# Performance work log

Hardware: AMD Instinct MI355X
Metric: run time of the kernel (lower is better)

## Reference

```python
import jax, jax.numpy as jnp
import numpy as np

B, D, H = 2048, 64, 512  # batch, state dim, vf hidden dim
IS_DIFFUSION = True      # vf output divided by 2.0 as in CNF.forward


def setup_inputs() -> dict:
    key = jax.random.key(0)
    ks = jax.random.split(key, 8)

    def lin(k, fi, fo):
        return jax.random.normal(k, (fi, fo), jnp.float32) / np.float32(np.sqrt(fi))

    return {
        "t": jax.random.uniform(ks[0], (1,), jnp.float32),      # scalar time, kept as [1]
        "x": jax.random.normal(ks[1], (B, D + 1), jnp.float32),  # last col = logp channel
        "W1": lin(ks[2], D + 1, H),
        "b1": jax.random.normal(ks[3], (H,), jnp.float32) * 0.01,
        "W2": lin(ks[4], H, H),
        "b2": jax.random.normal(ks[5], (H,), jnp.float32) * 0.01,
        "W3": lin(ks[6], H, D),
        "b3": jax.random.normal(ks[7], (D,), jnp.float32) * 0.01,
    }


def reference(t, x, W1, b1, W2, b2, W3, b3):
    scale = 2.0 if IS_DIFFUSION else 1.0
    xd = x[..., :-1]  # [B, D] -- drop augmented log-density channel

    def vf_single(xi):  # R^D -> R^D vector field, t and params closed over
        h = jnp.concatenate([xi, t])           # [D+1] (time-conditioned input)
        h = jnp.tanh(h @ W1 + b1)
        h = jnp.tanh(h @ W2 + b2)
        return (h @ W3 + b3) / scale

    dx = jax.vmap(vf_single)(xd)  # [B, D]
    # exact divergence: trace of per-sample Jacobian via reverse-mode (matches torch jacrev)
    div = jax.vmap(lambda xi: jnp.trace(jax.jacrev(vf_single)(xi)))(xd)  # [B]
    return jnp.concatenate([dx, div[:, None]], axis=-1)  # [B, D+1]
```

## Files before the change

kernel.cpp:

```cpp
#include <hip/hip_runtime.h>


constexpr int HD = 512;
constexpr int DD = 64;
constexpr int SB = 8;
constexpr int NB = 2048 / SB;

typedef __attribute__((ext_vector_type(8))) short bf16x8;
typedef __attribute__((ext_vector_type(4))) float f32x4;

__device__ inline unsigned short f2bf(float f) {
    union { float f; unsigned u; } v; v.f = f;
    return (unsigned short)((v.u + 0x7fffu + ((v.u >> 16) & 1u)) >> 16);
}
__device__ inline float fast_tanh(float xx) {
    float e = __expf(2.f * xx);
    return 1.f - 2.f / (e + 1.f);
}

__global__ __launch_bounds__(64) void cnf_pack_kernel(
    const float* __restrict__ W1, const float* __restrict__ W2,
    const float* __restrict__ W3, unsigned short* __restrict__ Bpack)
{
    __shared__ float w1s[64][33];
    __shared__ float w3s[16][65];
    const int b = blockIdx.x;
    const int mat = b >> 9, t = (b >> 4) & 31, kk = b & 15;
    const int l = threadIdx.x;
    const int q = l >> 4, nl = l & 15;
    const int n = t * 16 + nl;
    unsigned short o[8];
    if (mat == 0) {
#pragma unroll
        for (int j = 0; j < 8; ++j) {
            int k = kk * 32 + q * 8 + j;
            o[j] = f2bf(W2[k * HD + n]);
        }
    } else {
        for (int e = l; e < 64 * 32; e += 64) {
            int i = e >> 5, kl = e & 31;
            w1s[i][kl] = W1[i * HD + kk * 32 + kl];
        }
        for (int e = l; e < 16 * 64; e += 64) {
            int nn = e >> 6, i = e & 63;
            w3s[nn][i] = W3[(t * 16 + nn) * DD + i];
        }
        __syncthreads();
#pragma unroll
        for (int j = 0; j < 8; ++j) {
            int kl = q * 8 + j;
            float m = 0.f;
#pragma unroll 8
            for (int i = 0; i < 64; ++i) m += w1s[i][kl] * w3s[nl][i];
            o[j] = f2bf(W2[(kk * 32 + kl) * HD + n] * m);
        }
    }
    uint4 pk;
    pk.x = (unsigned)o[0] | ((unsigned)o[1] << 16);
    pk.y = (unsigned)o[2] | ((unsigned)o[3] << 16);
    pk.z = (unsigned)o[4] | ((unsigned)o[5] << 16);
    pk.w = (unsigned)o[6] | ((unsigned)o[7] << 16);
    reinterpret_cast<uint4*>(Bpack)[b * 64 + l] = pk;
}

__global__ __launch_bounds__(512, 2) void cnf_fused_kernel(
    const float* __restrict__ tptr, const float* __restrict__ x,
    const float* __restrict__ W1, const float* __restrict__ b1,
    const float* __restrict__ b2v, const float* __restrict__ W3,
    const float* __restrict__ b3, const unsigned short* __restrict__ Bpack,
    float* __restrict__ out)
{
    __shared__ float4 xsv[65 * 2];
    __shared__ unsigned short A_lds[16][520];
    __shared__ float4 h2v[HD * 2];
    __shared__ float4 divred[8][2];
    __shared__ float sm_b2[HD];

    const int tid  = threadIdx.x;
    const int s0   = blockIdx.x * SB;
    const int wave = tid >> 6, lane = tid & 63;

    {
        const float tval = tptr[0];
        for (int e = tid; e < SB * 65; e += 512) {
            int s = e / 65, i = e % 65;
            reinterpret_cast<float*>(xsv)[i * SB + s] =
                (i == DD) ? tval : x[(s0 + s) * 65 + i];
        }
        sm_b2[tid] = b2v[tid];
    }
    __syncthreads();

    {
        const int u = tid;
        const float bb = b1[u];
        float2 a0 = {bb, bb}, a1 = {bb, bb}, a2 = {bb, bb}, a3 = {bb, bb};
        for (int ib = 0; ib < 64; ib += 8) {
            float w[8];
#pragma unroll
            for (int qq = 0; qq < 8; ++qq) w[qq] = W1[(ib + qq) * HD + u];
#pragma unroll
            for (int qq = 0; qq < 8; ++qq) {
                float4 p = xsv[2 * (ib + qq)], r = xsv[2 * (ib + qq) + 1];
                a0.x += p.x * w[qq]; a0.y += p.y * w[qq];
                a1.x += p.z * w[qq]; a1.y += p.w * w[qq];
                a2.x += r.x * w[qq]; a2.y += r.y * w[qq];
                a3.x += r.z * w[qq]; a3.y += r.w * w[qq];
            }
        }
        {
            float w = W1[64 * HD + u];
            float4 p = xsv[128], r = xsv[129];
            a0.x += p.x * w; a0.y += p.y * w;
            a1.x += p.z * w; a1.y += p.w * w;
            a2.x += r.x * w; a2.y += r.y * w;
            a3.x += r.z * w; a3.y += r.w * w;
        }
        float h[8] = {fast_tanh(a0.x), fast_tanh(a0.y), fast_tanh(a1.x), fast_tanh(a1.y),
                      fast_tanh(a2.x), fast_tanh(a2.y), fast_tanh(a3.x), fast_tanh(a3.y)};
#pragma unroll
        for (int s = 0; s < 8; ++s) {
            A_lds[s][u]     = f2bf(h[s]);
            A_lds[8 + s][u] = f2bf(1.f - h[s] * h[s]);
        }
    }
    __syncthreads();

    f32x4 cw[4], cg[4];
#pragma unroll
    for (int i = 0; i < 4; ++i) { cw[i] = (f32x4){0,0,0,0}; cg[i] = (f32x4){0,0,0,0}; }
    {
        const unsigned short* arow = &A_lds[lane & 15][0];
        const int aoff = (lane >> 4) * 8;
        const bf16x8* bw = reinterpret_cast<const bf16x8*>(Bpack)
                         + (size_t)(wave * 64) * 64 + lane;
        const bf16x8* bg = bw + 32768;

        bf16x8 pA[16], pB[16];
        auto loadSB = [&](bf16x8* d, int kk) {
#pragma unroll
            for (int i = 0; i < 4; ++i) {
                d[i]      = bw[kk * 64 + i * 1024];
                d[4 + i]  = bg[kk * 64 + i * 1024];
                d[8 + i]  = bw[(kk + 1) * 64 + i * 1024];
                d[12 + i] = bg[(kk + 1) * 64 + i * 1024];
            }
        };
        auto mfmaSB = [&](const bf16x8* d, int kk) {
            bf16x8 af0 = *reinterpret_cast<const bf16x8*>(arow + kk * 32 + aoff);
#pragma unroll
            for (int i = 0; i < 4; ++i)
                cw[i] = __builtin_amdgcn_mfma_f32_16x16x32_bf16(af0, d[i], cw[i], 0, 0, 0);
#pragma unroll
            for (int i = 0; i < 4; ++i)
                cg[i] = __builtin_amdgcn_mfma_f32_16x16x32_bf16(af0, d[4 + i], cg[i], 0, 0, 0);
            bf16x8 af1 = *reinterpret_cast<const bf16x8*>(arow + (kk + 1) * 32 + aoff);
#pragma unroll
            for (int i = 0; i < 4; ++i)
                cw[i] = __builtin_amdgcn_mfma_f32_16x16x32_bf16(af1, d[8 + i], cw[i], 0, 0, 0);
#pragma unroll
            for (int i = 0; i < 4; ++i)
                cg[i] = __builtin_amdgcn_mfma_f32_16x16x32_bf16(af1, d[12 + i], cg[i], 0, 0, 0);
        };

        loadSB(pA, 0);
#pragma unroll
        for (int kb = 0; kb < 8; ++kb) {
            bf16x8* cur = (kb & 1) ? pB : pA;
            bf16x8* nxt = (kb & 1) ? pA : pB;
            if (kb < 7) loadSB(nxt, (kb + 1) * 2);
            mfmaSB(cur, kb * 2);
        }
    }

    {
        const int q = lane >> 4;
        const int src = (lane >= 32) ? lane - 32 : lane;
        float4 dp = {0.f, 0.f, 0.f, 0.f};
#pragma unroll
        for (int i = 0; i < 4; ++i) {
            const int m = wave * 64 + i * 16 + (lane & 15);
            const float bb = sm_b2[m];
            float4 hv;
            hv.x = fast_tanh(cw[i][0] + bb);
            hv.y = fast_tanh(cw[i][1] + bb);
            hv.z = fast_tanh(cw[i][2] + bb);
            hv.w = fast_tanh(cw[i][3] + bb);
            if (lane < 32) h2v[2 * m + q] = hv;
            float h0 = __shfl(hv.x, src), h1s = __shfl(hv.y, src);
            float h2s = __shfl(hv.z, src), h3s = __shfl(hv.w, src);
            dp.x += cg[i][0] * (1.f - h0 * h0);
            dp.y += cg[i][1] * (1.f - h1s * h1s);
            dp.z += cg[i][2] * (1.f - h2s * h2s);
            dp.w += cg[i][3] * (1.f - h3s * h3s);
        }
        if (lane >= 32) {
#pragma unroll
            for (int off = 8; off > 0; off >>= 1) {
                dp.x += __shfl_down(dp.x, off, 16);
                dp.y += __shfl_down(dp.y, off, 16);
                dp.z += __shfl_down(dp.z, off, 16);
                dp.w += __shfl_down(dp.w, off, 16);
            }
            if ((lane & 15) == 0) divred[wave][q - 2] = dp;
        }
    }
    __syncthreads();

    float* opart = reinterpret_cast<float*>(A_lds);

    {
        const int k = lane, part = wave;
        float o[8];
#pragma unroll
        for (int q = 0; q < 8; ++q) o[q] = 0.f;
        const int mb = part * 64;
        for (int mm = 0; mm < 64; mm += 4) {
            float w[4];
#pragma unroll
            for (int q = 0; q < 4; ++q) w[q] = W3[(mb + mm + q) * DD + k];
#pragma unroll
            for (int q = 0; q < 4; ++q) {
                const int m = mb + mm + q;
                float4 ha = h2v[2 * m], hb = h2v[2 * m + 1];
                o[0] += ha.x * w[q]; o[1] += ha.y * w[q];
                o[2] += ha.z * w[q]; o[3] += ha.w * w[q];
                o[4] += hb.x * w[q]; o[5] += hb.y * w[q];
                o[6] += hb.z * w[q]; o[7] += hb.w * w[q];
            }
        }
#pragma unroll
        for (int q = 0; q < 8; ++q) opart[part * 512 + q * 64 + k] = o[q];
    }
    __syncthreads();

    {
        const int s = tid >> 6, k = tid & 63;
        float sum = b3[k];
#pragma unroll
        for (int p = 0; p < 8; ++p) sum += opart[p * 512 + s * 64 + k];
        out[(s0 + s) * 65 + k] = 0.5f * sum;
    }
    if (tid < 8) {
        const int qq = tid >> 2, r = tid & 3;
        float ds = 0.f;
#pragma unroll
        for (int w = 0; w < 8; ++w)
            ds += reinterpret_cast<const float*>(&divred[w][qq])[r];
        out[(s0 + tid) * 65 + DD] = 0.5f * ds;
    }
}

extern "C" void kernel_launch(void* const* d_in, const int* in_sizes, int n_in,
                              void* d_out, int out_size, void* d_ws, size_t ws_size,
                              hipStream_t stream) {
    const float* t  = (const float*)d_in[0];
    const float* x  = (const float*)d_in[1];
    const float* W1 = (const float*)d_in[2];
    const float* b1 = (const float*)d_in[3];
    const float* W2 = (const float*)d_in[4];
    const float* b2 = (const float*)d_in[5];
    const float* W3 = (const float*)d_in[6];
    const float* b3 = (const float*)d_in[7];
    float* out = (float*)d_out;
    unsigned short* Bpack = (unsigned short*)d_ws;

    cnf_pack_kernel<<<1024, 64, 0, stream>>>(W1, W2, W3, Bpack);
    cnf_fused_kernel<<<NB, 512, 0, stream>>>(t, x, W1, b1, b2, W3, b3, Bpack, out);
}
```

Baseline: 97.85 us.

## Split fused CNF kernel into prep, pack, tiled GEMM and epilogue kernels

Result: slower. 105.6 us (+7.9%).

```diff
diff --git a/kernel.cpp b/kernel.cpp
--- a/kernel.cpp
+++ b/kernel.cpp
@@ -4,7 +4,6 @@
 constexpr int HD = 512;
 constexpr int DD = 64;
 constexpr int SB = 8;
-constexpr int NB = 2048 / SB;
 
 typedef __attribute__((ext_vector_type(8))) short bf16x8;
 typedef __attribute__((ext_vector_type(4))) float f32x4;
@@ -18,80 +17,28 @@
     return 1.f - 2.f / (e + 1.f);
 }
 
-__global__ __launch_bounds__(64) void cnf_pack_kernel(
-    const float* __restrict__ W1, const float* __restrict__ W2,
-    const float* __restrict__ W3, unsigned short* __restrict__ Bpack)
-{
-    __shared__ float w1s[64][33];
-    __shared__ float w3s[16][65];
-    const int b = blockIdx.x;
-    const int mat = b >> 9, t = (b >> 4) & 31, kk = b & 15;
-    const int l = threadIdx.x;
-    const int q = l >> 4, nl = l & 15;
-    const int n = t * 16 + nl;
-    unsigned short o[8];
-    if (mat == 0) {
-#pragma unroll
-        for (int j = 0; j < 8; ++j) {
-            int k = kk * 32 + q * 8 + j;
-            o[j] = f2bf(W2[k * HD + n]);
-        }
-    } else {
-        for (int e = l; e < 64 * 32; e += 64) {
-            int i = e >> 5, kl = e & 31;
-            w1s[i][kl] = W1[i * HD + kk * 32 + kl];
-        }
-        for (int e = l; e < 16 * 64; e += 64) {
-            int nn = e >> 6, i = e & 63;
-            w3s[nn][i] = W3[(t * 16 + nn) * DD + i];
-        }
-        __syncthreads();
-#pragma unroll
-        for (int j = 0; j < 8; ++j) {
-            int kl = q * 8 + j;
-            float m = 0.f;
-#pragma unroll 8
-            for (int i = 0; i < 64; ++i) m += w1s[i][kl] * w3s[nl][i];
-            o[j] = f2bf(W2[(kk * 32 + kl) * HD + n] * m);
-        }
-    }
-    uint4 pk;
-    pk.x = (unsigned)o[0] | ((unsigned)o[1] << 16);
-    pk.y = (unsigned)o[2] | ((unsigned)o[3] << 16);
-    pk.z = (unsigned)o[4] | ((unsigned)o[5] << 16);
-    pk.w = (unsigned)o[6] | ((unsigned)o[7] << 16);
-    reinterpret_cast<uint4*>(Bpack)[b * 64 + l] = pk;
-}
-
-__global__ __launch_bounds__(512, 2) void cnf_fused_kernel(
+__global__ __launch_bounds__(512) void cnf_prep_kernel(
     const float* __restrict__ tptr, const float* __restrict__ x,
     const float* __restrict__ W1, const float* __restrict__ b1,
-    const float* __restrict__ b2v, const float* __restrict__ W3,
-    const float* __restrict__ b3, const unsigned short* __restrict__ Bpack,
-    float* __restrict__ out)
+    const float* __restrict__ W3,
+    unsigned short* __restrict__ Apack,
+    float* __restrict__ Mws)
 {
     __shared__ float4 xsv[65 * 2];
-    __shared__ unsigned short A_lds[16][520];
-    __shared__ float4 h2v[HD * 2];
-    __shared__ float4 divred[8][2];
-    __shared__ float sm_b2[HD];
-
-    const int tid  = threadIdx.x;
-    const int s0   = blockIdx.x * SB;
-    const int wave = tid >> 6, lane = tid & 63;
-
-    {
-        const float tval = tptr[0];
-        for (int e = tid; e < SB * 65; e += 512) {
-            int s = e / 65, i = e % 65;
-            reinterpret_cast<float*>(xsv)[i * SB + s] =
-                (i == DD) ? tval : x[(s0 + s) * 65 + i];
-        }
-        sm_b2[tid] = b2v[tid];
-    }
-    __syncthreads();
-
-    {
+    __shared__ float w1b[64][8];
+    const int tid = threadIdx.x;
+
+    if (blockIdx.x < 256) {
+        const int s0 = blockIdx.x * SB;
+        {
+            const float tval = tptr[0];
+            for (int e = tid; e < SB * 65; e += 512) {
+                int s = e / 65, i = e % 65;
+                reinterpret_cast<float*>(xsv)[i * SB + s] =
+                    (i == DD) ? tval : x[(s0 + s) * 65 + i];
+            }
+        }
+        __syncthreads();
         const int u = tid;
         const float bb = b1[u];
         float2 a0 = {bb, bb}, a1 = {bb, bb}, a2 = {bb, bb}, a3 = {bb, bb};
@@ -118,96 +65,175 @@
         }
         float h[8] = {fast_tanh(a0.x), fast_tanh(a0.y), fast_tanh(a1.x), fast_tanh(a1.y),
                       fast_tanh(a2.x), fast_tanh(a2.y), fast_tanh(a3.x), fast_tanh(a3.y)};
+        unsigned short* Ah = Apack;
+        unsigned short* Ad = Apack + (size_t)2048 * HD;
 #pragma unroll
         for (int s = 0; s < 8; ++s) {
-            A_lds[s][u]     = f2bf(h[s]);
-            A_lds[8 + s][u] = f2bf(1.f - h[s] * h[s]);
+            Ah[(size_t)(s0 + s) * HD + u] = f2bf(h[s]);
+            Ad[(size_t)(s0 + s) * HD + u] = f2bf(1.f - h[s] * h[s]);
+        }
+    } else {
+        const int kb = (blockIdx.x - 256) * 8;
+        {
+            int i = tid >> 3, kq = tid & 7;
+            w1b[i][kq] = W1[i * HD + kb + kq];
+        }
+        __syncthreads();
+        const int n = tid;
+        float m8[8] = {0.f, 0.f, 0.f, 0.f, 0.f, 0.f, 0.f, 0.f};
+        for (int i = 0; i < 64; i += 4) {
+            float4 w3v = *reinterpret_cast<const float4*>(W3 + n * DD + i);
+#pragma unroll
+            for (int q = 0; q < 4; ++q) {
+                float wv = (q == 0) ? w3v.x : (q == 1) ? w3v.y : (q == 2) ? w3v.z : w3v.w;
+                float4 a = *reinterpret_cast<const float4*>(&w1b[i + q][0]);
+                float4 c = *reinterpret_cast<const float4*>(&w1b[i + q][4]);
+                m8[0] += a.x * wv; m8[1] += a.y * wv; m8[2] += a.z * wv; m8[3] += a.w * wv;
+                m8[4] += c.x * wv; m8[5] += c.y * wv; m8[6] += c.z * wv; m8[7] += c.w * wv;
+            }
+        }
+#pragma unroll
+        for (int j = 0; j < 8; ++j) Mws[(size_t)(kb + j) * HD + n] = m8[j];
+    }
+}
+
+__global__ __launch_bounds__(512) void cnf_pack_kernel(
+    const float* __restrict__ W2, const float* __restrict__ Mws,
+    unsigned short* __restrict__ Bpack)
+{
+    const int b = blockIdx.x * 8 + (threadIdx.x >> 6);
+    const int mat = b >> 9, t = (b >> 4) & 31, kk = b & 15;
+    const int l = threadIdx.x & 63;
+    const int q = l >> 4, nl = l & 15;
+    const int n = t * 16 + nl;
+    unsigned short o[8];
+#pragma unroll
+    for (int j = 0; j < 8; ++j) {
+        int k = kk * 32 + q * 8 + j;
+        float w = W2[k * HD + n];
+        if (mat) w *= Mws[(size_t)k * HD + n];
+        o[j] = f2bf(w);
+    }
+    uint4 pk;
+    pk.x = (unsigned)o[0] | ((unsigned)o[1] << 16);
+    pk.y = (unsigned)o[2] | ((unsigned)o[3] << 16);
+    pk.z = (unsigned)o[4] | ((unsigned)o[5] << 16);
+    pk.w = (unsigned)o[6] | ((unsigned)o[7] << 16);
+    reinterpret_cast<uint4*>(Bpack)[b * 64 + l] = pk;
+}
+
+__global__ __launch_bounds__(256) void cnf_gemm_kernel(
+    const unsigned short* __restrict__ Apack,
+    const unsigned short* __restrict__ Bpack,
+    float* __restrict__ C)
+{
+    const int b = blockIdx.x;
+    const int g  = b >> 7;
+    const int rt = (b >> 3) & 15;
+    const int ct = b & 7;
+    const int tid = threadIdx.x, wave = tid >> 6, lane = tid & 63;
+    const int row0 = rt * 128 + wave * 32;
+
+    const bf16x8* A  = reinterpret_cast<const bf16x8*>(Apack) + (size_t)g * 2048 * 64;
+    const bf16x8* Bf = reinterpret_cast<const bf16x8*>(Bpack)
+                     + (size_t)((g * 32 + ct * 4) * 16) * 64 + lane;
+    const int a0 = (row0 + (lane & 15)) * 64 + (lane >> 4);
+    const int a1 = a0 + 16 * 64;
+
+    f32x4 acc[2][4];
+#pragma unroll
+    for (int rg = 0; rg < 2; ++rg)
+#pragma unroll
+        for (int i = 0; i < 4; ++i) acc[rg][i] = (f32x4){0.f, 0.f, 0.f, 0.f};
+
+    bf16x8 p0[12], p1[12], p2[12];
+    auto loadSB = [&](bf16x8* d, int kk) {
+        d[0] = A[a0 + kk * 4];
+        d[1] = A[a1 + kk * 4];
+#pragma unroll
+        for (int i = 0; i < 4; ++i) d[2 + i] = Bf[(i * 16 + kk) * 64];
+        d[6] = A[a0 + (kk + 1) * 4];
+        d[7] = A[a1 + (kk + 1) * 4];
+#pragma unroll
+        for (int i = 0; i < 4; ++i) d[8 + i] = Bf[(i * 16 + kk + 1) * 64];
+    };
+    auto mfmaSB = [&](const bf16x8* d) {
+#pragma unroll
+        for (int i = 0; i < 4; ++i) {
+            acc[0][i] = __builtin_amdgcn_mfma_f32_16x16x32_bf16(d[0], d[2 + i], acc[0][i], 0, 0, 0);
+            acc[1][i] = __builtin_amdgcn_mfma_f32_16x16x32_bf16(d[1], d[2 + i], acc[1][i], 0, 0, 0);
+        }
+#pragma unroll
+        for (int i = 0; i < 4; ++i) {
+            acc[0][i] = __builtin_amdgcn_mfma_f32_16x16x32_bf16(d[6], d[8 + i], acc[0][i], 0, 0, 0);
+            acc[1][i] = __builtin_amdgcn_mfma_f32_16x16x32_bf16(d[7], d[8 + i], acc[1][i], 0, 0, 0);
+        }
+    };
+
+    loadSB(p0, 0);
+    loadSB(p1, 2);
+#pragma unroll
+    for (int kb = 0; kb < 8; ++kb) {
+        const int c3 = kb % 3, n3 = (kb + 2) % 3;
+        bf16x8* cur = (c3 == 0) ? p0 : (c3 == 1) ? p1 : p2;
+        bf16x8* nxt = (n3 == 0) ? p0 : (n3 == 1) ? p1 : p2;
+        if (kb < 6) loadSB(nxt, (kb + 2) * 2);
+        mfmaSB(cur);
+    }
+
+    float* Cg = C + (size_t)g * 2048 * HD;
+    const int colb = ct * 64 + (lane & 15);
+#pragma unroll
+    for (int rg = 0; rg < 2; ++rg) {
+        const int rbase = row0 + rg * 16 + (lane >> 4) * 4;
+#pragma unroll
+        for (int i = 0; i < 4; ++i) {
+#pragma unroll
+            for (int reg = 0; reg < 4; ++reg)
+                Cg[(size_t)(rbase + reg) * HD + colb + i * 16] = acc[rg][i][reg];
+        }
+    }
+}
+
+__global__ __launch_bounds__(512) void cnf_out_kernel(
+    const float* __restrict__ C,
+    const float* __restrict__ b2v, const float* __restrict__ W3,
+    const float* __restrict__ b3, float* __restrict__ out)
+{
+    __shared__ float4 h2v[HD * 2];
+    __shared__ float opart[8 * 512];
+    __shared__ float divred[8][8];
+    const int tid = threadIdx.x;
+    const int s0 = blockIdx.x * SB;
+    const int wave = tid >> 6, lane = tid & 63;
+    const float* C1 = C;
+    const float* C2 = C + (size_t)2048 * HD;
+
+    {
+        const int m = tid;
+        const float bb = b2v[m];
+        float hh[8], dp[8];
+#pragma unroll
+        for (int s = 0; s < 8; ++s) {
+            float c1 = C1[(size_t)(s0 + s) * HD + m];
+            float c2 = C2[(size_t)(s0 + s) * HD + m];
+            float h = fast_tanh(c1 + bb);
+            hh[s] = h;
+            dp[s] = c2 * (1.f - h * h);
+        }
+        h2v[2 * m]     = (float4){hh[0], hh[1], hh[2], hh[3]};
+        h2v[2 * m + 1] = (float4){hh[4], hh[5], hh[6], hh[7]};
+#pragma unroll
+        for (int s = 0; s < 8; ++s) {
+#pragma unroll
+            for (int off = 32; off > 0; off >>= 1) dp[s] += __shfl_down(dp[s], off);
+        }
+        if (lane == 0) {
+#pragma unroll
+            for (int s = 0; s < 8; ++s) divred[wave][s] = dp[s];
         }
     }
     __syncthreads();
-
-    f32x4 cw[4], cg[4];
-#pragma unroll
-    for (int i = 0; i < 4; ++i) { cw[i] = (f32x4){0,0,0,0}; cg[i] = (f32x4){0,0,0,0}; }
-    {
-        const unsigned short* arow = &A_lds[lane & 15][0];
-        const int aoff = (lane >> 4) * 8;
-        const bf16x8* bw = reinterpret_cast<const bf16x8*>(Bpack)
-                         + (size_t)(wave * 64) * 64 + lane;
-        const bf16x8* bg = bw + 32768;
-
-        bf16x8 pA[16], pB[16];
-        auto loadSB = [&](bf16x8* d, int kk) {
-#pragma unroll
-            for (int i = 0; i < 4; ++i) {
-                d[i]      = bw[kk * 64 + i * 1024];
-                d[4 + i]  = bg[kk * 64 + i * 1024];
-                d[8 + i]  = bw[(kk + 1) * 64 + i * 1024];
-                d[12 + i] = bg[(kk + 1) * 64 + i * 1024];
-            }
-        };
-        auto mfmaSB = [&](const bf16x8* d, int kk) {
-            bf16x8 af0 = *reinterpret_cast<const bf16x8*>(arow + kk * 32 + aoff);
-#pragma unroll
-            for (int i = 0; i < 4; ++i)
-                cw[i] = __builtin_amdgcn_mfma_f32_16x16x32_bf16(af0, d[i], cw[i], 0, 0, 0);
-#pragma unroll
-            for (int i = 0; i < 4; ++i)
-                cg[i] = __builtin_amdgcn_mfma_f32_16x16x32_bf16(af0, d[4 + i], cg[i], 0, 0, 0);
-            bf16x8 af1 = *reinterpret_cast<const bf16x8*>(arow + (kk + 1) * 32 + aoff);
-#pragma unroll
-            for (int i = 0; i < 4; ++i)
-                cw[i] = __builtin_amdgcn_mfma_f32_16x16x32_bf16(af1, d[8 + i], cw[i], 0, 0, 0);
-#pragma unroll
-            for (int i = 0; i < 4; ++i)
-                cg[i] = __builtin_amdgcn_mfma_f32_16x16x32_bf16(af1, d[12 + i], cg[i], 0, 0, 0);
-        };
-
-        loadSB(pA, 0);
-#pragma unroll
-        for (int kb = 0; kb < 8; ++kb) {
-            bf16x8* cur = (kb & 1) ? pB : pA;
-            bf16x8* nxt = (kb & 1) ? pA : pB;
-            if (kb < 7) loadSB(nxt, (kb + 1) * 2);
-            mfmaSB(cur, kb * 2);
-        }
-    }
-
-    {
-        const int q = lane >> 4;
-        const int src = (lane >= 32) ? lane - 32 : lane;
-        float4 dp = {0.f, 0.f, 0.f, 0.f};
-#pragma unroll
-        for (int i = 0; i < 4; ++i) {
-            const int m = wave * 64 + i * 16 + (lane & 15);
-            const float bb = sm_b2[m];
-            float4 hv;
-            hv.x = fast_tanh(cw[i][0] + bb);
-            hv.y = fast_tanh(cw[i][1] + bb);
-            hv.z = fast_tanh(cw[i][2] + bb);
-            hv.w = fast_tanh(cw[i][3] + bb);
-            if (lane < 32) h2v[2 * m + q] = hv;
-            float h0 = __shfl(hv.x, src), h1s = __shfl(hv.y, src);
-            float h2s = __shfl(hv.z, src), h3s = __shfl(hv.w, src);
-            dp.x += cg[i][0] * (1.f - h0 * h0);
-            dp.y += cg[i][1] * (1.f - h1s * h1s);
-            dp.z += cg[i][2] * (1.f - h2s * h2s);
-            dp.w += cg[i][3] * (1.f - h3s * h3s);
-        }
-        if (lane >= 32) {
-#pragma unroll
-            for (int off = 8; off > 0; off >>= 1) {
-                dp.x += __shfl_down(dp.x, off, 16);
-                dp.y += __shfl_down(dp.y, off, 16);
-                dp.z += __shfl_down(dp.z, off, 16);
-                dp.w += __shfl_down(dp.w, off, 16);
-            }
-            if ((lane & 15) == 0) divred[wave][q - 2] = dp;
-        }
-    }
-    __syncthreads();
-
-    float* opart = reinterpret_cast<float*>(A_lds);
 
     {
         const int k = lane, part = wave;
@@ -242,11 +268,9 @@
         out[(s0 + s) * 65 + k] = 0.5f * sum;
     }
     if (tid < 8) {
-        const int qq = tid >> 2, r = tid & 3;
         float ds = 0.f;
 #pragma unroll
-        for (int w = 0; w < 8; ++w)
-            ds += reinterpret_cast<const float*>(&divred[w][qq])[r];
+        for (int w = 0; w < 8; ++w) ds += divred[w][tid];
         out[(s0 + tid) * 65 + DD] = 0.5f * ds;
     }
 }
@@ -263,8 +287,14 @@
     const float* W3 = (const float*)d_in[6];
     const float* b3 = (const float*)d_in[7];
     float* out = (float*)d_out;
+
     unsigned short* Bpack = (unsigned short*)d_ws;
-
-    cnf_pack_kernel<<<1024, 64, 0, stream>>>(W1, W2, W3, Bpack);
-    cnf_fused_kernel<<<NB, 512, 0, stream>>>(t, x, W1, b1, b2, W3, b3, Bpack, out);
-}
+    float*          Mws   = (float*)((char*)d_ws + (1 << 20));
+    unsigned short* Apack = (unsigned short*)((char*)d_ws + (2 << 20));
+    float*          Cws   = (float*)((char*)d_ws + (6 << 20));
+
+    cnf_prep_kernel<<<320, 512, 0, stream>>>(t, x, W1, b1, W3, Apack, Mws);
+    cnf_pack_kernel<<<128, 512, 0, stream>>>(W2, Mws, Bpack);
+    cnf_gemm_kernel<<<256, 256, 0, stream>>>(Apack, Bpack, Cws);
+    cnf_out_kernel<<<256, 512, 0, stream>>>(Cws, b2, W3, b3, out);
+}
```

## Merge weight-packing kernel into main kernel with cooperative grid sync

Applied to the files above, without the earlier changes.

Measured after the change: 193.6 us. 97.9% more time.

```diff
diff --git a/kernel.cpp b/kernel.cpp
--- a/kernel.cpp
+++ b/kernel.cpp
@@ -1,4 +1,7 @@
 #include <hip/hip_runtime.h>
+#include <hip/hip_cooperative_groups.h>
+
+namespace cg = cooperative_groups;
 
 
 constexpr int HD = 512;
@@ -18,67 +21,28 @@
     return 1.f - 2.f / (e + 1.f);
 }
 
-__global__ __launch_bounds__(64) void cnf_pack_kernel(
-    const float* __restrict__ W1, const float* __restrict__ W2,
-    const float* __restrict__ W3, unsigned short* __restrict__ Bpack)
-{
-    __shared__ float w1s[64][33];
-    __shared__ float w3s[16][65];
-    const int b = blockIdx.x;
-    const int mat = b >> 9, t = (b >> 4) & 31, kk = b & 15;
-    const int l = threadIdx.x;
-    const int q = l >> 4, nl = l & 15;
-    const int n = t * 16 + nl;
-    unsigned short o[8];
-    if (mat == 0) {
-#pragma unroll
-        for (int j = 0; j < 8; ++j) {
-            int k = kk * 32 + q * 8 + j;
-            o[j] = f2bf(W2[k * HD + n]);
-        }
-    } else {
-        for (int e = l; e < 64 * 32; e += 64) {
-            int i = e >> 5, kl = e & 31;
-            w1s[i][kl] = W1[i * HD + kk * 32 + kl];
-        }
-        for (int e = l; e < 16 * 64; e += 64) {
-            int nn = e >> 6, i = e & 63;
-            w3s[nn][i] = W3[(t * 16 + nn) * DD + i];
-        }
-        __syncthreads();
-#pragma unroll
-        for (int j = 0; j < 8; ++j) {
-            int kl = q * 8 + j;
-            float m = 0.f;
-#pragma unroll 8
-            for (int i = 0; i < 64; ++i) m += w1s[i][kl] * w3s[nl][i];
-            o[j] = f2bf(W2[(kk * 32 + kl) * HD + n] * m);
-        }
-    }
-    uint4 pk;
-    pk.x = (unsigned)o[0] | ((unsigned)o[1] << 16);
-    pk.y = (unsigned)o[2] | ((unsigned)o[3] << 16);
-    pk.z = (unsigned)o[4] | ((unsigned)o[5] << 16);
-    pk.w = (unsigned)o[6] | ((unsigned)o[7] << 16);
-    reinterpret_cast<uint4*>(Bpack)[b * 64 + l] = pk;
-}
-
-__global__ __launch_bounds__(512, 2) void cnf_fused_kernel(
+
+__global__ __launch_bounds__(512, 2) void cnf_mega_kernel(
     const float* __restrict__ tptr, const float* __restrict__ x,
     const float* __restrict__ W1, const float* __restrict__ b1,
-    const float* __restrict__ b2v, const float* __restrict__ W3,
-    const float* __restrict__ b3, const unsigned short* __restrict__ Bpack,
-    float* __restrict__ out)
+    const float* __restrict__ W2, const float* __restrict__ b2v,
+    const float* __restrict__ W3, const float* __restrict__ b3,
+    unsigned short* Bpack, float* __restrict__ out)
 {
     __shared__ float4 xsv[65 * 2];
     __shared__ unsigned short A_lds[16][520];
     __shared__ float4 h2v[HD * 2];
     __shared__ float4 divred[8][2];
     __shared__ float sm_b2[HD];
+    __shared__ float w1s[64][65];
+    __shared__ float w3s[16][68];
 
     const int tid  = threadIdx.x;
-    const int s0   = blockIdx.x * SB;
+    const int bidx = blockIdx.x;
+    const int s0   = bidx * SB;
     const int wave = tid >> 6, lane = tid & 63;
+    const int kbase = ((2 * bidx) & 15) * 32;
+    const int tG    = (2 * bidx) >> 4;
 
     {
         const float tval = tptr[0];
@@ -88,8 +52,56 @@
                 (i == DD) ? tval : x[(s0 + s) * 65 + i];
         }
         sm_b2[tid] = b2v[tid];
+        for (int e = tid; e < 64 * 64; e += 512) {
+            int i = e >> 6, k = e & 63;
+            w1s[i][k] = W1[i * HD + kbase + k];
+        }
+        for (int e = tid; e < 16 * 64; e += 512) {
+            int nn = e >> 6, i = e & 63;
+            w3s[nn][i] = W3[(tG * 16 + nn) * DD + i];
+        }
     }
     __syncthreads();
+
+    if (wave >= 2 && wave < 6) {
+        const int q = lane >> 4, nl = lane & 15;
+        unsigned short o[8];
+        int c;
+        if (wave >= 4) {
+            c = 2 * bidx + (wave - 4);
+            const int t = (c >> 4) & 31, kk = c & 15;
+            const int n = t * 16 + nl;
+#pragma unroll
+            for (int j = 0; j < 8; ++j)
+                o[j] = f2bf(W2[(kk * 32 + q * 8 + j) * HD + n]);
+        } else {
+            const int u = wave - 2;
+            c = 512 + 2 * bidx + u;
+            const int kk = (2 * bidx + u) & 15;
+            const int n = tG * 16 + nl;
+            float w3r[64];
+#pragma unroll
+            for (int i4 = 0; i4 < 16; ++i4) {
+                float4 v = *reinterpret_cast<const float4*>(&w3s[nl][i4 * 4]);
+                w3r[i4 * 4]     = v.x; w3r[i4 * 4 + 1] = v.y;
+                w3r[i4 * 4 + 2] = v.z; w3r[i4 * 4 + 3] = v.w;
+            }
+#pragma unroll
+            for (int j = 0; j < 8; ++j) {
+                const int kloc = u * 32 + q * 8 + j;
+                float m = 0.f;
+#pragma unroll 8
+                for (int i = 0; i < 64; ++i) m += w1s[i][kloc] * w3r[i];
+                o[j] = f2bf(W2[(kk * 32 + q * 8 + j) * HD + n] * m);
+            }
+        }
+        uint4 pk;
+        pk.x = (unsigned)o[0] | ((unsigned)o[1] << 16);
+        pk.y = (unsigned)o[2] | ((unsigned)o[3] << 16);
+        pk.z = (unsigned)o[4] | ((unsigned)o[5] << 16);
+        pk.w = (unsigned)o[6] | ((unsigned)o[7] << 16);
+        reinterpret_cast<uint4*>(Bpack)[c * 64 + lane] = pk;
+    }
 
     {
         const int u = tid;
@@ -124,11 +136,13 @@
             A_lds[8 + s][u] = f2bf(1.f - h[s] * h[s]);
         }
     }
-    __syncthreads();
-
-    f32x4 cw[4], cg[4];
-#pragma unroll
-    for (int i = 0; i < 4; ++i) { cw[i] = (f32x4){0,0,0,0}; cg[i] = (f32x4){0,0,0,0}; }
+
+    __threadfence();
+    cg::this_grid().sync();
+
+    f32x4 cw[4], cg_[4];
+#pragma unroll
+    for (int i = 0; i < 4; ++i) { cw[i] = (f32x4){0,0,0,0}; cg_[i] = (f32x4){0,0,0,0}; }
     {
         const unsigned short* arow = &A_lds[lane & 15][0];
         const int aoff = (lane >> 4) * 8;
@@ -153,14 +167,14 @@
                 cw[i] = __builtin_amdgcn_mfma_f32_16x16x32_bf16(af0, d[i], cw[i], 0, 0, 0);
 #pragma unroll
             for (int i = 0; i < 4; ++i)
-                cg[i] = __builtin_amdgcn_mfma_f32_16x16x32_bf16(af0, d[4 + i], cg[i], 0, 0, 0);
+                cg_[i] = __builtin_amdgcn_mfma_f32_16x16x32_bf16(af0, d[4 + i], cg_[i], 0, 0, 0);
             bf16x8 af1 = *reinterpret_cast<const bf16x8*>(arow + (kk + 1) * 32 + aoff);
 #pragma unroll
             for (int i = 0; i < 4; ++i)
                 cw[i] = __builtin_amdgcn_mfma_f32_16x16x32_bf16(af1, d[8 + i], cw[i], 0, 0, 0);
 #pragma unroll
             for (int i = 0; i < 4; ++i)
-                cg[i] = __builtin_amdgcn_mfma_f32_16x16x32_bf16(af1, d[12 + i], cg[i], 0, 0, 0);
+                cg_[i] = __builtin_amdgcn_mfma_f32_16x16x32_bf16(af1, d[12 + i], cg_[i], 0, 0, 0);
         };
 
         loadSB(pA, 0);
@@ -189,10 +203,10 @@
             if (lane < 32) h2v[2 * m + q] = hv;
             float h0 = __shfl(hv.x, src), h1s = __shfl(hv.y, src);
             float h2s = __shfl(hv.z, src), h3s = __shfl(hv.w, src);
-            dp.x += cg[i][0] * (1.f - h0 * h0);
-            dp.y += cg[i][1] * (1.f - h1s * h1s);
-            dp.z += cg[i][2] * (1.f - h2s * h2s);
-            dp.w += cg[i][3] * (1.f - h3s * h3s);
+            dp.x += cg_[i][0] * (1.f - h0 * h0);
+            dp.y += cg_[i][1] * (1.f - h1s * h1s);
+            dp.z += cg_[i][2] * (1.f - h2s * h2s);
+            dp.w += cg_[i][3] * (1.f - h3s * h3s);
         }
         if (lane >= 32) {
 #pragma unroll
@@ -265,6 +279,8 @@
     float* out = (float*)d_out;
     unsigned short* Bpack = (unsigned short*)d_ws;
 
-    cnf_pack_kernel<<<1024, 64, 0, stream>>>(W1, W2, W3, Bpack);
-    cnf_fused_kernel<<<NB, 512, 0, stream>>>(t, x, W1, b1, b2, W3, b3, Bpack, out);
-}
+    void* args[] = {(void*)&t,  (void*)&x,  (void*)&W1, (void*)&b1, (void*)&W2,
+                    (void*)&b2, (void*)&W3, (void*)&b3, (void*)&Bpack, (void*)&out};
+    hipLaunchCooperativeKernel((const void*)cnf_mega_kernel, dim3(NB), dim3(512),
+                               args, 0, stream);
+}
```
